# Optimization experiments

Measured on AMD Instinct MI355X. Metric: run time of the kernel, lower is better.

The kernel has to match this reference:

```python
import jax, jax.numpy as jnp
import numpy as np

H = 8          # query heads
KVH = 1        # key/value heads
HD = 256       # head dim
ROPE_BASE = 10000.0


def _rotate_half(x):
    x1, x2 = x[..., : HD // 2], x[..., HD // 2 :]
    return jnp.concatenate((-x2, x1), axis=-1)


def _rope_cos_sin(position_ids):
    # position_ids: [B, S] int -> cos/sin: [B, S, HD]
    inv_freq = 1.0 / (ROPE_BASE ** (jnp.arange(0, HD, 2, dtype=jnp.float32) / HD))
    freqs = position_ids.astype(jnp.float32)[..., None] * inv_freq  # [B,S,HD/2]
    emb = jnp.concatenate((freqs, freqs), axis=-1)                  # [B,S,HD]
    return jnp.cos(emb), jnp.sin(emb)


def setup_inputs() -> dict:
    key = jax.random.key(0)
    ks = jax.random.split(key, 5)
    B, S, D = 2, 2048, 2048
    return {
        "hidden_states": jax.random.normal(ks[0], (B, S, D), dtype=jnp.float32),
        "attention_mask": jnp.zeros((B, 1, S, S), dtype=jnp.float32),
        "position_ids": jnp.broadcast_to(jnp.arange(S, dtype=jnp.int32), (B, S)),
        "Wq": jax.random.normal(ks[1], (D, H * HD), dtype=jnp.float32) * 0.02,
        "Wk": jax.random.normal(ks[2], (D, KVH * HD), dtype=jnp.float32) * 0.02,
        "Wv": jax.random.normal(ks[3], (D, KVH * HD), dtype=jnp.float32) * 0.02,
        "Wo": jax.random.normal(ks[4], (H * HD, D), dtype=jnp.float32) * 0.02,
    }


def reference(hidden_states, attention_mask, position_ids, Wq, Wk, Wv, Wo):
    B, S, D = hidden_states.shape
    # projections -> [B, heads, S, HD]
    q = jnp.einsum("bsd,df->bsf", hidden_states, Wq).reshape(B, S, H, HD).transpose(0, 2, 1, 3)
    k = jnp.einsum("bsd,df->bsf", hidden_states, Wk).reshape(B, S, KVH, HD).transpose(0, 2, 1, 3)
    v = jnp.einsum("bsd,df->bsf", hidden_states, Wv).reshape(B, S, KVH, HD).transpose(0, 2, 1, 3)

    cos, sin = _rope_cos_sin(position_ids)
    cos, sin = cos[:, None], sin[:, None]  # unsqueeze head dim
    q = q * cos + _rotate_half(q) * sin
    k = k * cos + _rotate_half(k) * sin

    # GQA: repeat kv heads to match query heads
    rep = H // KVH
    k = jnp.repeat(k, rep, axis=1)
    v = jnp.repeat(v, rep, axis=1)

    d_k = D // H  # matches torch code's scaling (== HD here)
    scores = jnp.einsum("bhqd,bhkd->bhqk", q, k) / jnp.sqrt(jnp.float32(d_k))
    scores = scores + attention_mask
    attn = jax.nn.softmax(scores, axis=-1)  # dropout p=0 / eval mode

    out = jnp.einsum("bhqk,bhkd->bhqd", attn, v)  # [B,H,S,HD]
    out = out.transpose(0, 2, 1, 3).reshape(B, S, H * HD)
    out = jnp.einsum("bsf,fd->bsd", out, Wo)
    return out
```

## Files before the change

### kernel.cpp

```cpp
#include <hip/hip_runtime.h>
#include <cmath>


typedef __bf16 bf16;
typedef __attribute__((ext_vector_type(8))) __bf16 bf16x8;
typedef __attribute__((ext_vector_type(4))) __bf16 bf16x4;
typedef __attribute__((ext_vector_type(4))) float f32x4;

#define S_LEN 2048
#define D_MODEL 2048
#define H_NUM 8
#define HDIM 256
#define NT (S_LEN / 64)
#define SM_BIAS 8.0f

#define BAR __builtin_amdgcn_s_barrier()
#define SCHED0 __builtin_amdgcn_sched_barrier(0)

__device__ __forceinline__ void gl_lds16(const bf16* g, bf16* l) {
  __builtin_amdgcn_global_load_lds(
      (const __attribute__((address_space(1))) void*)g,
      (__attribute__((address_space(3))) void*)l, 16, 0, 0);
}

__global__ void cvt_bf16(const float* __restrict__ src, bf16* __restrict__ dst) {
  const int i = (blockIdx.x * 256 + threadIdx.x) * 4;
  const float4 v = *(const float4*)(src + i);
  bf16x4 o;
  o[0] = (bf16)v.x; o[1] = (bf16)v.y; o[2] = (bf16)v.z; o[3] = (bf16)v.w;
  *(bf16x4*)(dst + i) = o;
}

__global__ void tpose_all(const float* __restrict__ Wq, const float* __restrict__ Wk,
                          const float* __restrict__ Wv, const float* __restrict__ Wo,
                          bf16* __restrict__ Wqkvt, bf16* __restrict__ Wot) {
  __shared__ float t[32][33];
  const int tx = threadIdx.x, ty = threadIdx.y;
  const int bx = blockIdx.x;
  const int k0 = blockIdx.y * 32;
  const float* W; bf16* Wt; int Ncols, no0, n0;
  if (bx < 64)      { W = Wq; Wt = Wqkvt; Ncols = 2048; no0 = 0;    n0 = bx * 32; }
  else if (bx < 72) { W = Wk; Wt = Wqkvt; Ncols = 256;  no0 = 2048; n0 = (bx - 64) * 32; }
  else if (bx < 80) { W = Wv; Wt = Wqkvt; Ncols = 256;  no0 = 2304; n0 = (bx - 72) * 32; }
  else              { W = Wo; Wt = Wot;   Ncols = 2048; no0 = 0;    n0 = (bx - 80) * 32; }
#pragma unroll
  for (int i = 0; i < 4; ++i)
    t[ty + 8 * i][tx] = W[(size_t)(k0 + ty + 8 * i) * Ncols + (n0 + tx)];
  __syncthreads();
#pragma unroll
  for (int i = 0; i < 4; ++i)
    Wt[(size_t)(no0 + n0 + ty + 8 * i) * D_MODEL + (k0 + tx)] = (bf16)t[tx][ty + 8 * i];
}

__global__ __launch_bounds__(512, 2)
void gemm_bf16(const bf16* __restrict__ A, const bf16* __restrict__ Wt,
               bf16* __restrict__ Cq, bf16* __restrict__ Ck, bf16* __restrict__ Cv,
               float* __restrict__ Cf, int NX, int mode) {
  __shared__ bf16 As[2][2][128 * 64];
  __shared__ bf16 Bs[2][2][128 * 64];
  const int tid = threadIdx.x;
  const int lane = tid & 63;
  const int w = tid >> 6;
  const int c16 = lane & 15;
  const int quad = lane >> 4;
  const int wm = w >> 2;
  const int wn = w & 3;

  const int nwg = gridDim.x;
  const int swz = (blockIdx.x & 7) * (nwg >> 3) + (blockIdx.x >> 3);
  const int m0 = (swz / NX) * 256;
  const int n0 = (swz % NX) * 256;

  const char* Ab = (const char*)A;
  const char* Bb = (const char*)Wt;
  const int lr8 = lane >> 3;
  const int scb = ((lane & 7) ^ lr8) << 4;

  f32x4 acc[8][4];
#pragma unroll
  for (int i = 0; i < 8; ++i)
#pragma unroll
    for (int j = 0; j < 4; ++j)
#pragma unroll
      for (int r = 0; r < 4; ++r) acc[i][j][r] = 0.f;

  auto stg = [&](const char* gcol, int grow0, bf16* lhalf) {
#pragma unroll
    for (int j2 = 0; j2 < 2; ++j2) {
      const int c = w * 2 + j2;
      gl_lds16((const bf16*)(gcol + (size_t)(grow0 + c * 8 + lr8) * 4096 + scb),
               lhalf + c * 512);
    }
  };
  auto ldA = [&](int sl, int qm, bf16x8* d) {
    const char* base = (const char*)&As[sl][wm][0];
#pragma unroll
    for (int i = 0; i < 4; ++i) {
      const int row = qm * 64 + i * 16 + c16;
      const int sw = (row & 7) << 4;
#pragma unroll
      for (int kk = 0; kk < 2; ++kk)
        d[i * 2 + kk] = *(const bf16x8*)(base + row * 128 + ((kk * 64 + quad * 16) ^ sw));
    }
  };
  auto ldB = [&](int sl, int qn, bf16x8* d) {
    const char* base = (const char*)&Bs[sl][wn >> 1][0];
#pragma unroll
    for (int j = 0; j < 2; ++j) {
      const int row = (wn & 1) * 64 + qn * 32 + j * 16 + c16;
      const int sw = (row & 7) << 4;
#pragma unroll
      for (int kk = 0; kk < 2; ++kk)
        d[j * 2 + kk] = *(const bf16x8*)(base + row * 128 + ((kk * 64 + quad * 16) ^ sw));
    }
  };
  auto mm = [&](int qm, int qn, const bf16x8* a, const bf16x8* bb) {
    __builtin_amdgcn_s_setprio(1);
#pragma unroll
    for (int kk = 0; kk < 2; ++kk)
#pragma unroll
      for (int i = 0; i < 4; ++i)
#pragma unroll
        for (int j = 0; j < 2; ++j)
          acc[qm * 4 + i][qn * 2 + j] = __builtin_amdgcn_mfma_f32_16x16x32_bf16(
              a[i * 2 + kk], bb[j * 2 + kk], acc[qm * 4 + i][qn * 2 + j], 0, 0, 0);
    __builtin_amdgcn_s_setprio(0);
  };

  bf16x8 Xa[8], Ya[8], Xb[4], Yb[4];

  stg(Ab, m0, &As[0][0][0]);        stg(Ab, m0 + 128, &As[0][1][0]);
  stg(Bb, n0, &Bs[0][0][0]);        stg(Bb, n0 + 128, &Bs[0][1][0]);
  stg(Bb + 128, n0, &Bs[1][0][0]);  stg(Bb + 128, n0 + 128, &Bs[1][1][0]);
  asm volatile("s_waitcnt vmcnt(4)" ::: "memory");
  BAR;

  for (int t = 0; t < 16; ++t) {
    const int kc = t * 256;
    const bool pf = (t < 15);
    ldA(0, 0, Xa); ldB(0, 0, Xb);
    stg(Ab + kc + 128, m0, &As[1][0][0]);
    BAR; mm(0, 0, Xa, Xb);
    ldB(0, 1, Yb);
    stg(Ab + kc + 128, m0 + 128, &As[1][1][0]);
    BAR; mm(0, 1, Xa, Yb);
    ldA(0, 1, Ya);
    if (pf) stg(Bb + kc + 256, n0, &Bs[0][0][0]);
    BAR; mm(1, 1, Ya, Yb);
    if (pf) {
      stg(Ab + kc + 256, m0, &As[0][0][0]);
      asm volatile("s_waitcnt vmcnt(4)" ::: "memory");
    } else {
      asm volatile("s_waitcnt vmcnt(0)" ::: "memory");
    }
    BAR; mm(1, 0, Ya, Xb);
    ldA(1, 0, Xa); ldB(1, 0, Xb);
    if (pf) stg(Bb + kc + 256, n0 + 128, &Bs[0][1][0]);
    BAR; mm(0, 0, Xa, Xb);
    ldB(1, 1, Yb);
    if (pf) stg(Ab + kc + 256, m0 + 128, &As[0][1][0]);
    BAR; mm(0, 1, Xa, Yb);
    ldA(1, 1, Ya);
    if (pf) stg(Bb + kc + 384, n0, &Bs[1][0][0]);
    BAR; mm(1, 1, Ya, Yb);
    if (pf) {
      stg(Bb + kc + 384, n0 + 128, &Bs[1][1][0]);
      asm volatile("s_waitcnt vmcnt(4)" ::: "memory");
      BAR; mm(1, 0, Ya, Xb);
    } else {
      BAR; mm(1, 0, Ya, Xb);
    }
  }

#pragma unroll
  for (int i = 0; i < 8; ++i)
#pragma unroll
    for (int j = 0; j < 4; ++j) {
      const int n = n0 + wn * 64 + j * 16 + c16;
#pragma unroll
      for (int r = 0; r < 4; ++r) {
        const int m = m0 + wm * 128 + i * 16 + quad * 4 + r;
        const float val = acc[i][j][r];
        if (mode == 1) {
          const int b = m >> 11, s = m & 2047;
          if (n0 < 2048) {
            const int h = n >> 8, hd = n & 255;
            Cq[((((size_t)b * H_NUM + h) * S_LEN + s) << 8) + hd] = (bf16)val;
          } else if (n0 < 2304) {
            Ck[((size_t)m << 8) + (n - 2048)] = (bf16)val;
          } else {
            Cv[((size_t)((b << 8) + (n - 2304)) << 11) + s] = (bf16)val;
          }
        } else {
          Cf[(size_t)m * D_MODEL + n] = val;
        }
      }
    }
}

#define ROPE_C (-0.07195578415606394f)

__global__ void rope_all(bf16* __restrict__ q, bf16* __restrict__ k,
                         const int* __restrict__ pos, int BHS) {
  const int idx = blockIdx.x * 256 + threadIdx.x;
  const int j = idx & 127;
  const int t = idx >> 7;
  float sn, cs;
  if (t < BHS) {
    const int s = t & 2047;
    const int b = t >> 14;
    const float p = (float)pos[(b << 11) + s];
    sincosf(p * expf((float)j * ROPE_C), &sn, &cs);
    bf16* base = q + ((size_t)t << 8);
    const float x1 = (float)base[j], x2 = (float)base[j + 128];
    base[j] = (bf16)(x1 * cs - x2 * sn);
    base[j + 128] = (bf16)(x2 * cs + x1 * sn);
  } else {
    const int t2 = t - BHS;
    const int s = t2 & 2047;
    const int b = t2 >> 11;
    const float p = (float)pos[(b << 11) + s];
    sincosf(p * expf((float)j * ROPE_C), &sn, &cs);
    bf16* base = k + ((size_t)t2 << 8);
    const float x1 = (float)base[j], x2 = (float)base[j + 128];
    base[j] = (bf16)(x1 * cs - x2 * sn);
    base[j + 128] = (bf16)(x2 * cs + x1 * sn);
  }
}

__global__ __launch_bounds__(512, 2)
void flash_bf16(const bf16* __restrict__ qg, const bf16* __restrict__ kg,
                const bf16* __restrict__ vg, const float* __restrict__ msk,
                bf16* __restrict__ ao) {
  __shared__ bf16 Ks[2][64 * 256];
  __shared__ bf16 Vs[2][256 * 64];
  __shared__ bf16 Ps[128 * 64];
  __shared__ float Lp[2][128];

  const int tid = threadIdx.x;
  const int lane = tid & 63;
  const int w = tid >> 6;
  const int c16 = lane & 15;
  const int quad = lane >> 4;
  const int qi = w & 3;
  const int sec = w >> 2;

  const int bidx = blockIdx.x;
  int b, qb;
  if (gridDim.x == 256) {
    b = (bidx & 7) >> 2;
    qb = ((bidx & 3) << 5) | (bidx >> 3);
  } else {
    b = bidx >> 7;
    qb = bidx & 127;
  }
  const int q0 = qb * 16;

  const bf16* qh = qg + ((((size_t)b * H_NUM + qi * 2) * S_LEN + q0) << 8);
  const char* kbase = (const char*)(kg + ((size_t)b << 19));
  const char* vbase = (const char*)(vg + ((size_t)b << 19));
  const float* mbase = msk + (size_t)b * S_LEN * S_LEN + (size_t)q0 * S_LEN;

  bf16x8 qf[2][8];
#pragma unroll
  for (int mi = 0; mi < 2; ++mi)
#pragma unroll
    for (int kd = 0; kd < 8; ++kd)
      qf[mi][kd] = *(const bf16x8*)&qh[(((size_t)mi * S_LEN + c16) << 8) + kd * 32 + quad * 8];

  f32x4 oacc[2][8];
#pragma unroll
  for (int mi = 0; mi < 2; ++mi)
#pragma unroll
    for (int nj = 0; nj < 8; ++nj)
#pragma unroll
      for (int r = 0; r < 4; ++r) oacc[mi][nj][r] = 0.f;
  float plsum[2][4];
#pragma unroll
  for (int mi = 0; mi < 2; ++mi)
#pragma unroll
    for (int r = 0; r < 4; ++r) plsum[mi][r] = 0.f;

  auto stage = [&](int k0, int buf) {
#pragma unroll
    for (int j = 0; j < 4; ++j) {
      const int ki = w * 4 + j;
      const int krow = ki * 2 + (lane >> 5);
      const int kcb = ((lane & 31) * 16) ^ ((krow & 7) << 4);
      gl_lds16((const bf16*)(kbase + ((size_t)(k0 + krow) << 9) + kcb),
               &Ks[buf][ki * 512]);
      const int vrow = ki * 8 + (lane >> 3);
      const int vcb = ((lane & 7) * 16) ^ ((vrow & 7) << 4);
      gl_lds16((const bf16*)(vbase + ((size_t)vrow << 12) + (k0 << 1) + vcb),
               &Vs[buf][ki * 512]);
    }
  };

  stage(0, 0);
  __syncthreads();

  for (int t = 0; t < NT; ++t) {
    const int k0 = t * 64;
    const int buf = t & 1;
    if (t + 1 < NT) stage(k0 + 64, buf ^ 1);

    float ml[2][4];
#pragma unroll
    for (int nj = 0; nj < 2; ++nj)
#pragma unroll
      for (int r = 0; r < 4; ++r)
        ml[nj][r] = mbase[(size_t)(quad * 4 + r) * S_LEN +
                          k0 + sec * 32 + nj * 16 + c16];

    f32x4 sc[2][2];
#pragma unroll
    for (int mi = 0; mi < 2; ++mi)
#pragma unroll
      for (int nj = 0; nj < 2; ++nj)
#pragma unroll
        for (int r = 0; r < 4; ++r) sc[mi][nj][r] = 0.f;
    __builtin_amdgcn_s_setprio(1);
#pragma unroll
    for (int kd = 0; kd < 8; ++kd) {
      bf16x8 bK[2];
#pragma unroll
      for (int nj = 0; nj < 2; ++nj) {
        const int row = sec * 32 + nj * 16 + c16;
        bK[nj] = *(const bf16x8*)((const char*)&Ks[buf][0] + row * 512 +
                                  ((kd * 64 + quad * 16) ^ ((row & 7) << 4)));
      }
#pragma unroll
      for (int mi = 0; mi < 2; ++mi)
#pragma unroll
        for (int nj = 0; nj < 2; ++nj)
          sc[mi][nj] = __builtin_amdgcn_mfma_f32_16x16x32_bf16(qf[mi][kd], bK[nj], sc[mi][nj], 0, 0, 0);
    }
    __builtin_amdgcn_s_setprio(0);

#pragma unroll
    for (int mi = 0; mi < 2; ++mi)
#pragma unroll
      for (int nj = 0; nj < 2; ++nj)
#pragma unroll
        for (int r = 0; r < 4; ++r) {
          const float p = __expf(sc[mi][nj][r] * 0.0625f + ml[nj][r] - SM_BIAS);
          plsum[mi][r] += p;
          const int row = qi * 32 + mi * 16 + quad * 4 + r;
          const int cb = ((sec * 32 + nj * 16 + c16) * 2) ^ ((row & 7) << 4);
          *(bf16*)((char*)&Ps[0] + row * 128 + cb) = (bf16)p;
        }

    SCHED0;
    asm volatile("s_waitcnt lgkmcnt(0)" ::: "memory");
    BAR;
    SCHED0;

    bf16x8 pa[2][2];
#pragma unroll
    for (int mi = 0; mi < 2; ++mi)
#pragma unroll
      for (int ks = 0; ks < 2; ++ks) {
        const int row = qi * 32 + mi * 16 + c16;
        pa[mi][ks] = *(const bf16x8*)((const char*)&Ps[0] + row * 128 +
                                      ((ks * 64 + quad * 16) ^ ((row & 7) << 4)));
      }
    __builtin_amdgcn_s_setprio(1);
#pragma unroll
    for (int nj = 0; nj < 8; ++nj) {
#pragma unroll
      for (int ks = 0; ks < 2; ++ks) {
        const int drow = sec * 128 + nj * 16 + c16;
        const bf16x8 bv = *(const bf16x8*)((const char*)&Vs[buf][0] + drow * 128 +
                                           ((ks * 64 + quad * 16) ^ ((drow & 7) << 4)));
#pragma unroll
        for (int mi = 0; mi < 2; ++mi)
          oacc[mi][nj] = __builtin_amdgcn_mfma_f32_16x16x32_bf16(pa[mi][ks], bv, oacc[mi][nj], 0, 0, 0);
      }
    }
    __builtin_amdgcn_s_setprio(0);

    __syncthreads();
  }

#pragma unroll
  for (int mi = 0; mi < 2; ++mi)
#pragma unroll
    for (int r = 0; r < 4; ++r) {
      float s = plsum[mi][r];
      s += __shfl_xor(s, 1, 64);
      s += __shfl_xor(s, 2, 64);
      s += __shfl_xor(s, 4, 64);
      s += __shfl_xor(s, 8, 64);
      if (c16 == 0) Lp[sec][qi * 32 + mi * 16 + quad * 4 + r] = s;
    }
  __syncthreads();
  float li[2][4];
#pragma unroll
  for (int mi = 0; mi < 2; ++mi)
#pragma unroll
    for (int r = 0; r < 4; ++r) {
      const int row = qi * 32 + mi * 16 + quad * 4 + r;
      li[mi][r] = 1.f / (Lp[0][row] + Lp[1][row]);
    }
  bf16* obase = ao + (size_t)(b * S_LEN + q0 + quad * 4) * D_MODEL + qi * 512 + sec * 128;
#pragma unroll
  for (int mi = 0; mi < 2; ++mi)
#pragma unroll
    for (int nj = 0; nj < 8; ++nj)
#pragma unroll
      for (int r = 0; r < 4; ++r)
        obase[(size_t)r * D_MODEL + mi * 256 + nj * 16 + c16] =
            (bf16)(oacc[mi][nj][r] * li[mi][r]);
}

extern "C" void kernel_launch(void* const* d_in, const int* in_sizes, int n_in,
                              void* d_out, int out_size, void* d_ws, size_t ws_size,
                              hipStream_t stream) {
  const float* hs   = (const float*)d_in[0];
  const float* mask = (const float*)d_in[1];
  const int*   pos  = (const int*)d_in[2];
  const float* Wq   = (const float*)d_in[3];
  const float* Wk   = (const float*)d_in[4];
  const float* Wv   = (const float*)d_in[5];
  const float* Wo   = (const float*)d_in[6];
  float* out = (float*)d_out;

  const int B = in_sizes[2] / S_LEN;
  const int M = B * S_LEN;

  char* wsc = (char*)d_ws;
  bf16* hsb = (bf16*)wsc;
  bf16* aob = hsb;
  size_t off = (size_t)M * D_MODEL * 2;
  bf16* Wqkvt = (bf16*)(wsc + off); off += (size_t)2560 * D_MODEL * 2;
  bf16* Wot   = (bf16*)(wsc + off); off += (size_t)D_MODEL * D_MODEL * 2;
  bf16* kb    = (bf16*)(wsc + off);
  bf16* vb    = kb + (size_t)M * HDIM;

  bf16* qb = (bf16*)d_out;

  const dim3 blk(256);
  cvt_bf16<<<(M * D_MODEL) / 1024, blk, 0, stream>>>(hs, hsb);
  tpose_all<<<dim3(144, 64), dim3(32, 8), 0, stream>>>(Wq, Wk, Wv, Wo, Wqkvt, Wot);

  gemm_bf16<<<10 * (M / 256), dim3(512), 0, stream>>>(hsb, Wqkvt, qb, kb, vb, nullptr, 10, 1);

  rope_all<<<(B * (H_NUM + 1) * S_LEN * 128) / 256, blk, 0, stream>>>(
      qb, kb, pos, B * H_NUM * S_LEN);

  flash_bf16<<<B * (S_LEN / 16), dim3(512), 0, stream>>>(qb, kb, vb, mask, aob);

  gemm_bf16<<<8 * (M / 256), dim3(512), 0, stream>>>(aob, Wot, nullptr, nullptr, nullptr, out, 8, 3);
}
```

Before: 373.6 us.

## Repartition flash attention waves into 2 row groups by 4 key quarters

Changes the per-wave work split in the flash attention kernel. Waves previously each owned 32 query rows by 32 keys for QK and 128 head-dim columns for PV. They now own 64 query rows (4 heads), 16 keys for QK and 64 head-dim columns for PV. Each K fragment loaded from LDS now feeds 4 MFMAs instead of 2, and each V fragment also feeds 4, which cuts LDS reads per MFMA at the cost of more Q-fragment registers (qf grows to 4x8). Row sums are now combined across four key-quarter partials instead of two.

```diff
diff --git a/kernel.cpp b/kernel.cpp
--- a/kernel.cpp
+++ b/kernel.cpp
@@ -235,15 +235,15 @@
   __shared__ bf16 Ks[2][64 * 256];
   __shared__ bf16 Vs[2][256 * 64];
   __shared__ bf16 Ps[128 * 64];
-  __shared__ float Lp[2][128];
+  __shared__ float Lp[4][128];
 
   const int tid = threadIdx.x;
   const int lane = tid & 63;
   const int w = tid >> 6;
   const int c16 = lane & 15;
   const int quad = lane >> 4;
-  const int qi = w & 3;
-  const int sec = w >> 2;
+  const int rg = w & 1;
+  const int kq = w >> 1;
 
   const int bidx = blockIdx.x;
   int b, qb;
@@ -256,28 +256,28 @@
   }
   const int q0 = qb * 16;
 
-  const bf16* qh = qg + ((((size_t)b * H_NUM + qi * 2) * S_LEN + q0) << 8);
+  const bf16* qh = qg + ((((size_t)b * H_NUM + rg * 4) * S_LEN + q0) << 8);
   const char* kbase = (const char*)(kg + ((size_t)b << 19));
   const char* vbase = (const char*)(vg + ((size_t)b << 19));
   const float* mbase = msk + (size_t)b * S_LEN * S_LEN + (size_t)q0 * S_LEN;
 
-  bf16x8 qf[2][8];
-#pragma unroll
-  for (int mi = 0; mi < 2; ++mi)
+  bf16x8 qf[4][8];
+#pragma unroll
+  for (int mi = 0; mi < 4; ++mi)
 #pragma unroll
     for (int kd = 0; kd < 8; ++kd)
       qf[mi][kd] = *(const bf16x8*)&qh[(((size_t)mi * S_LEN + c16) << 8) + kd * 32 + quad * 8];
 
-  f32x4 oacc[2][8];
-#pragma unroll
-  for (int mi = 0; mi < 2; ++mi)
-#pragma unroll
-    for (int nj = 0; nj < 8; ++nj)
+  f32x4 oacc[4][4];
+#pragma unroll
+  for (int mi = 0; mi < 4; ++mi)
+#pragma unroll
+    for (int nj = 0; nj < 4; ++nj)
 #pragma unroll
       for (int r = 0; r < 4; ++r) oacc[mi][nj][r] = 0.f;
-  float plsum[2][4];
-#pragma unroll
-  for (int mi = 0; mi < 2; ++mi)
+  float plsum[4][4];
+#pragma unroll
+  for (int mi = 0; mi < 4; ++mi)
 #pragma unroll
     for (int r = 0; r < 4; ++r) plsum[mi][r] = 0.f;
 
@@ -304,76 +304,63 @@
     const int buf = t & 1;
     if (t + 1 < NT) stage(k0 + 64, buf ^ 1);
 
-    float ml[2][4];
-#pragma unroll
-    for (int nj = 0; nj < 2; ++nj)
-#pragma unroll
-      for (int r = 0; r < 4; ++r)
-        ml[nj][r] = mbase[(size_t)(quad * 4 + r) * S_LEN +
-                          k0 + sec * 32 + nj * 16 + c16];
-
-    f32x4 sc[2][2];
-#pragma unroll
-    for (int mi = 0; mi < 2; ++mi)
-#pragma unroll
-      for (int nj = 0; nj < 2; ++nj)
-#pragma unroll
-        for (int r = 0; r < 4; ++r) sc[mi][nj][r] = 0.f;
+    float ml[4];
+#pragma unroll
+    for (int r = 0; r < 4; ++r)
+      ml[r] = mbase[(size_t)(quad * 4 + r) * S_LEN + k0 + kq * 16 + c16];
+
+    f32x4 sc[4];
+#pragma unroll
+    for (int mi = 0; mi < 4; ++mi)
+#pragma unroll
+      for (int r = 0; r < 4; ++r) sc[mi][r] = 0.f;
     __builtin_amdgcn_s_setprio(1);
 #pragma unroll
     for (int kd = 0; kd < 8; ++kd) {
-      bf16x8 bK[2];
-#pragma unroll
-      for (int nj = 0; nj < 2; ++nj) {
-        const int row = sec * 32 + nj * 16 + c16;
-        bK[nj] = *(const bf16x8*)((const char*)&Ks[buf][0] + row * 512 +
-                                  ((kd * 64 + quad * 16) ^ ((row & 7) << 4)));
+      const int row = kq * 16 + c16;
+      const bf16x8 bK = *(const bf16x8*)((const char*)&Ks[buf][0] + row * 512 +
+                                         ((kd * 64 + quad * 16) ^ ((row & 7) << 4)));
+#pragma unroll
+      for (int mi = 0; mi < 4; ++mi)
+        sc[mi] = __builtin_amdgcn_mfma_f32_16x16x32_bf16(qf[mi][kd], bK, sc[mi], 0, 0, 0);
+    }
+    __builtin_amdgcn_s_setprio(0);
+
+#pragma unroll
+    for (int mi = 0; mi < 4; ++mi)
+#pragma unroll
+      for (int r = 0; r < 4; ++r) {
+        const float p = __expf(sc[mi][r] * 0.0625f + ml[r] - SM_BIAS);
+        plsum[mi][r] += p;
+        const int row = rg * 64 + mi * 16 + quad * 4 + r;
+        const int cb = ((kq * 16 + c16) * 2) ^ ((row & 7) << 4);
+        *(bf16*)((char*)&Ps[0] + row * 128 + cb) = (bf16)p;
       }
-#pragma unroll
-      for (int mi = 0; mi < 2; ++mi)
-#pragma unroll
-        for (int nj = 0; nj < 2; ++nj)
-          sc[mi][nj] = __builtin_amdgcn_mfma_f32_16x16x32_bf16(qf[mi][kd], bK[nj], sc[mi][nj], 0, 0, 0);
-    }
-    __builtin_amdgcn_s_setprio(0);
-
-#pragma unroll
-    for (int mi = 0; mi < 2; ++mi)
-#pragma unroll
-      for (int nj = 0; nj < 2; ++nj)
-#pragma unroll
-        for (int r = 0; r < 4; ++r) {
-          const float p = __expf(sc[mi][nj][r] * 0.0625f + ml[nj][r] - SM_BIAS);
-          plsum[mi][r] += p;
-          const int row = qi * 32 + mi * 16 + quad * 4 + r;
-          const int cb = ((sec * 32 + nj * 16 + c16) * 2) ^ ((row & 7) << 4);
-          *(bf16*)((char*)&Ps[0] + row * 128 + cb) = (bf16)p;
-        }
 
     SCHED0;
     asm volatile("s_waitcnt lgkmcnt(0)" ::: "memory");
     BAR;
     SCHED0;
 
-    bf16x8 pa[2][2];
-#pragma unroll
-    for (int mi = 0; mi < 2; ++mi)
+    bf16x8 pa[4][2];
+#pragma unroll
+    for (int mi = 0; mi < 4; ++mi)
 #pragma unroll
       for (int ks = 0; ks < 2; ++ks) {
-        const int row = qi * 32 + mi * 16 + c16;
+        const int row = rg * 64 + mi * 16 + c16;
         pa[mi][ks] = *(const bf16x8*)((const char*)&Ps[0] + row * 128 +
                                       ((ks * 64 + quad * 16) ^ ((row & 7) << 4)));
       }
     __builtin_amdgcn_s_setprio(1);
 #pragma unroll
-    for (int nj = 0; nj < 8; ++nj) {
+    for (int nj = 0; nj < 4; ++nj) {
 #pragma unroll
       for (int ks = 0; ks < 2; ++ks) {
-        const int drow = sec * 128 + nj * 16 + c16;
+        const int drow = kq * 64 + nj * 16 + c16;
         const bf16x8 bv = *(const bf16x8*)((const char*)&Vs[buf][0] + drow * 128 +
                                            ((ks * 64 + quad * 16) ^ ((drow & 7) << 4)));
 #pragma unroll
-        for (int mi = 0; mi < 2; ++mi)
+        for (int mi = 0; mi < 4; ++mi)
           oacc[mi][nj] = __builtin_amdgcn_mfma_f32_16x16x32_bf16(pa[mi][ks], bv, oacc[mi][nj], 0, 0, 0);
       }
     }
@@ -383,7 +370,7 @@
   }
 
 #pragma unroll
-  for (int mi = 0; mi < 2; ++mi)
+  for (int mi = 0; mi < 4; ++mi)
 #pragma unroll
     for (int r = 0; r < 4; ++r) {
       float s = plsum[mi][r];
@@ -391,22 +378,23 @@
       s += __shfl_xor(s, 2, 64);
       s += __shfl_xor(s, 4, 64);
       s += __shfl_xor(s, 8, 64);
-      if (c16 == 0) Lp[sec][qi * 32 + mi * 16 + quad * 4 + r] = s;
+      if (c16 == 0) Lp[kq][rg * 64 + mi * 16 + quad * 4 + r] = s;
     }
   __syncthreads();
-  float li[2][4];
-#pragma unroll
-  for (int mi = 0; mi < 2; ++mi)
+  float li[4][4];
+#pragma unroll
+  for (int mi = 0; mi < 4; ++mi)
 #pragma unroll
     for (int r = 0; r < 4; ++r) {
-      const int row = qi * 32 + mi * 16 + quad * 4 + r;
-      li[mi][r] = 1.f / (Lp[0][row] + Lp[1][row]);
-    }
-  bf16* obase = ao + (size_t)(b * S_LEN + q0 + quad * 4) * D_MODEL + qi * 512 + sec * 128;
-#pragma unroll
-  for (int mi = 0; mi < 2; ++mi)
-#pragma unroll
-    for (int nj = 0; nj < 8; ++nj)
+      const int row = rg * 64 + mi * 16 + quad * 4 + r;
+      li[mi][r] = 1.f / (((Lp[0][row] + Lp[1][row]) + (Lp[2][row] + Lp[3][row])));
+    }
+  bf16* obase = ao + (size_t)(b * S_LEN + q0 + quad * 4) * D_MODEL +
+                rg * 1024 + kq * 64;
+#pragma unroll
+  for (int mi = 0; mi < 4; ++mi)
+#pragma unroll
+    for (int nj = 0; nj < 4; ++nj)
 #pragma unroll
       for (int r = 0; r < 4; ++r)
         obase[(size_t)r * D_MODEL + mi * 256 + nj * 16 + c16] =
```

Result: slower. 463.7 us (+24.1%).
